# Kernel optimization log

Measured on AMD Instinct MI355X. Metric: run time of the kernel, lower is better.

Reference implementation:

```python
import jax, jax.numpy as jnp
from jax import lax
import numpy as np

CHANNELS = 16
THRESH = 0.1
UPDATE_RATE = 0.25


def _sobel_kernel():
    ident = np.array([[0., 0., 0.], [0., 1., 0.], [0., 0., 0.]], np.float32)
    sx = np.array([[-1., 0., 1.], [-2., 0., 2.], [-1., 0., 1.]], np.float32)
    sy = sx.T
    k = np.stack([ident, sx, sy])[:, None, :, :]          # [3,1,3,3]
    k = np.tile(k, (CHANNELS, 1, 1, 1))                   # [48,1,3,3] (torch repeat order)
    return jnp.asarray(k)


def _perceive(x, w_sobel):
    # circular pad then depthwise grouped conv (groups=CHANNELS, 3 filters per group)
    xp = jnp.pad(x, ((0, 0), (0, 0), (1, 1), (1, 1)), mode='wrap')
    return lax.conv_general_dilated(
        xp, w_sobel, window_strides=(1, 1), padding='VALID',
        dimension_numbers=('NCHW', 'OIHW', 'NCHW'),
        feature_group_count=CHANNELS)                     # [B,48,H,W]


def _alive_mask(x):
    alpha = x[:, 3:4]                                     # [B,1,H,W]
    p = jnp.pad(alpha, ((0, 0), (0, 0), (1, 1), (1, 1)), mode='wrap')
    m = lax.reduce_window(p, -jnp.inf, lax.max, (1, 1, 3, 3), (1, 1, 1, 1), 'VALID')
    return (m > THRESH).astype(x.dtype)


def _mlp(y, w1, b1, w2, b2, w3):
    h = jax.nn.relu(jnp.einsum('bchw,oc->bohw', y, w1) + b1[None, :, None, None])
    h = jax.nn.relu(jnp.einsum('bchw,oc->bohw', h, w2) + b2[None, :, None, None])
    return jnp.einsum('bchw,oc->bohw', h, w3)             # [B,16,H,W], no bias


def setup_inputs() -> dict:
    key = jax.random.key(0)
    ks = jax.random.split(key, 7)
    B, H, W, steps = 8, 256, 256, 2
    s = 0.1
    return {
        'x': jax.random.uniform(ks[0], (B, CHANNELS, H, W), jnp.float32),
        'w1': jax.random.normal(ks[1], (64, 48), jnp.float32) * s,
        'b1': jax.random.normal(ks[2], (64,), jnp.float32) * s,
        'w2': jax.random.normal(ks[3], (64, 64), jnp.float32) * s,
        'b2': jax.random.normal(ks[4], (64,), jnp.float32) * s,
        'w3': jax.random.normal(ks[5], (CHANNELS, 64), jnp.float32) * s,
        'update_masks': jax.random.uniform(ks[6], (steps, B, 1, H, W), jnp.float32),
        'steps': steps,
    }


def reference(x, w1, b1, w2, b2, w3, update_masks, steps):
    w_sobel = _sobel_kernel()
    for i in range(steps):
        pre = _alive_mask(x)
        y = _mlp(_perceive(x, w_sobel), w1, b1, w2, b2, w3)
        um = (update_masks[i] < UPDATE_RATE).astype(x.dtype)
        x = x + y * um
        post = _alive_mask(x)
        x = x * (pre * post)
    return x
```

## Files before the change

### kernel.cpp

```cpp
#include <hip/hip_runtime.h>

#define NB 8
#define NC 16
#define NH 256
#define NW 256
#define ALIVE_THRESH 0.1f
#define UPDATE_RATE 0.25f

typedef __attribute__((ext_vector_type(8))) short bf16x8;
typedef __attribute__((ext_vector_type(4))) float f32x4;
typedef unsigned short ushort_t;

#define MFMA16(a, b, c) __builtin_amdgcn_mfma_f32_16x16x32_bf16((a), (b), (c), 0, 0, 0)

static __device__ __forceinline__ unsigned short f2bf(float f) {
    union { float f; unsigned u; } x; x.f = f;
    unsigned r = x.u + 0x7FFFu + ((x.u >> 16) & 1u);
    return (unsigned short)(r >> 16);
}
static __device__ __forceinline__ float bf2f(unsigned short b) {
    union { unsigned u; float f; } x; x.u = ((unsigned)b) << 16; return x.f;
}

static __device__ __forceinline__ int ybyte(int px, int g) {
    return px * 128 + ((g ^ (px & 7)) << 4);
}

__global__ void prep_weights(const float* __restrict__ w1, const float* __restrict__ b1,
                             const float* __restrict__ w2, const float* __restrict__ w3,
                             int4* __restrict__ wf)
{
    const int f = blockIdx.x, l = threadIdx.x;
    const int lq = l >> 4, ln = l & 15;
    union { unsigned short us[8]; int4 v; } u;
    if (f < 8) {
        const int mt = f >> 1, ks = f & 1, m = mt * 16 + ln;
        #pragma unroll
        for (int j = 0; j < 8; ++j) {
            const int k = ks * 32 + lq * 8 + j;
            float v = (k < 48) ? w1[m * 48 + k] : ((k == 48) ? b1[m] : 0.0f);
            u.us[j] = f2bf(v);
        }
    } else if (f < 16) {
        const int ff = f - 8, mt = ff >> 1, ks = ff & 1, m = mt * 16 + ln;
        #pragma unroll
        for (int j = 0; j < 8; ++j)
            u.us[j] = f2bf(w2[m * 64 + (ks * 32 + lq * 8 + j)]);
    } else {
        const int ks = f - 16, m = ln;
        #pragma unroll
        for (int j = 0; j < 8; ++j)
            u.us[j] = f2bf(w3[m * 64 + (ks * 32 + lq * 8 + j)]);
    }
    wf[f * 64 + l] = u.v;
}

template<bool MASK_IN, bool OUT_BF16>
__global__ __launch_bounds__(256) void nca_step_a(
    const void* __restrict__ xin_v,
    const float* __restrict__ um,
    const float* __restrict__ b2,
    const int4*  __restrict__ wf,
    void* __restrict__ xout_v,
    const unsigned char* __restrict__ preb_in,
    unsigned char* __restrict__ preb_out)
{
    __shared__ char      ybuf[256 * 128];
    __shared__ unsigned  sd[NC][NW];
    __shared__ float     premax2[NW];
    __shared__ float     mmid[NW];

    const int t = threadIdx.x;
    const int bx = blockIdx.x;
    const int h = ((bx & 7) << 5) | (bx >> 3);
    const int b = blockIdx.y;
    const int hm = (h - 1) & (NH - 1), hp = (h + 1) & (NH - 1);
    const size_t cs = (size_t)NH * NW;
    const size_t base = (size_t)b * NC * cs;

    float mreg[NC], dreg[NC];

    if constexpr (MASK_IN) {
        const ushort_t* xin = (const ushort_t*)xin_v;
        float* vbuf = (float*)ybuf;
        const ushort_t* ac = xin + base + 3 * cs;
        float am[5];
        #pragma unroll
        for (int j = 0; j < 5; ++j)
            am[j] = bf2f(ac[(size_t)((h - 2 + j) & (NH - 1)) * NW + t]);
        vbuf[0 * NW + t] = fmaxf(fmaxf(am[0], am[1]), am[2]);
        vbuf[1 * NW + t] = fmaxf(fmaxf(am[1], am[2]), am[3]);
        vbuf[2 * NW + t] = fmaxf(fmaxf(am[2], am[3]), am[4]);
        const unsigned char p0 = preb_in[((size_t)b * NH + hm) * NW + t];
        const unsigned char p1 = preb_in[((size_t)b * NH + h ) * NW + t];
        const unsigned char p2 = preb_in[((size_t)b * NH + hp) * NW + t];
        __syncthreads();

        const int tm = (t - 1) & (NW - 1), tp = (t + 1) & (NW - 1);
        float x0 = fmaxf(fmaxf(vbuf[tm],           vbuf[t]),           vbuf[tp]);
        float x1 = fmaxf(fmaxf(vbuf[NW + tm],      vbuf[NW + t]),      vbuf[NW + tp]);
        float x2 = fmaxf(fmaxf(vbuf[2 * NW + tm],  vbuf[2 * NW + t]),  vbuf[2 * NW + tp]);
        const float m0 = (x0 > ALIVE_THRESH && p0) ? 1.0f : 0.0f;
        const float m1 = (x1 > ALIVE_THRESH && p1) ? 1.0f : 0.0f;
        const float m2 = (x2 > ALIVE_THRESH && p2) ? 1.0f : 0.0f;
        mmid[t] = m1;
        premax2[t] = fmaxf(fmaxf(am[1] * m0, am[2] * m1), am[3] * m2);

        #pragma unroll
        for (int c = 0; c < NC; ++c) {
            float top, mid, bot;
            if (c == 3) { top = am[1] * m0; mid = am[2] * m1; bot = am[3] * m2; }
            else {
                const ushort_t* xc = xin + base + (size_t)c * cs;
                top = bf2f(xc[(size_t)hm * NW + t]) * m0;
                mid = bf2f(xc[(size_t)h  * NW + t]) * m1;
                bot = bf2f(xc[(size_t)hp * NW + t]) * m2;
            }
            float s = top + 2.0f * mid + bot, d = bot - top;
            sd[c][t] = (unsigned)f2bf(s) | ((unsigned)f2bf(d) << 16);
            mreg[c] = mid; dreg[c] = d;
        }
        __syncthreads();
    } else {
        const float* xin = (const float*)xin_v;
        #pragma unroll
        for (int c = 0; c < NC; ++c) {
            const float* xc = xin + base + (size_t)c * cs;
            float top = xc[(size_t)hm * NW + t];
            float mid = xc[(size_t)h  * NW + t];
            float bot = xc[(size_t)hp * NW + t];
            float s = top + 2.0f * mid + bot, d = bot - top;
            sd[c][t] = (unsigned)f2bf(s) | ((unsigned)f2bf(d) << 16);
            mreg[c] = mid; dreg[c] = d;
            if (c == 3) premax2[t] = fmaxf(fmaxf(top, mid), bot);
        }
        __syncthreads();
    }

    {
        const int tm = (t - 1) & (NW - 1), tp = (t + 1) & (NW - 1);
        float mx = fmaxf(fmaxf(premax2[tm], premax2[t]), premax2[tp]);
        preb_out[((size_t)b * NH + h) * NW + t] = (mx > ALIVE_THRESH) ? 1 : 0;
    }

    {
        unsigned yp[24];
        #pragma unroll
        for (int c = 0; c < NC; ++c) {
            unsigned L = sd[c][(t - 1) & (NW - 1)];
            unsigned R = sd[c][(t + 1) & (NW - 1)];
            float sl = bf2f((unsigned short)L), dl = bf2f((unsigned short)(L >> 16));
            float sr = bf2f((unsigned short)R), dr = bf2f((unsigned short)(R >> 16));
            float y0 = mreg[c];
            float y1 = sr - sl;
            float y2 = dl + 2.0f * dreg[c] + dr;
            unsigned short u[3] = { f2bf(y0), f2bf(y1), f2bf(y2) };
            #pragma unroll
            for (int q = 0; q < 3; ++q) {
                const int k = 3 * c + q;
                if ((k & 1) == 0) yp[k >> 1]  = u[q];
                else              yp[k >> 1] |= ((unsigned)u[q]) << 16;
            }
        }
        char* yb = (char*)ybuf;
        #pragma unroll
        for (int g = 0; g < 6; ++g) {
            union { unsigned w[4]; int4 v; } pk;
            pk.w[0] = yp[4 * g]; pk.w[1] = yp[4 * g + 1];
            pk.w[2] = yp[4 * g + 2]; pk.w[3] = yp[4 * g + 3];
            *(int4*)(yb + ybyte(t, g)) = pk.v;
        }
        int4 biasrow; biasrow.x = 0x3F80; biasrow.y = 0; biasrow.z = 0; biasrow.w = 0;
        *(int4*)(yb + ybyte(t, 6)) = biasrow;
        int4 zz; zz.x = zz.y = zz.z = zz.w = 0;
        *(int4*)(yb + ybyte(t, 7)) = zz;
    }

    char* yb = (char*)ybuf;
    const int lane = t & 63, wv = t >> 6;
    const int lq = lane >> 4, ln = lane & 15;
    const int px0 = wv * 64;

    float umv[4];
    {
        const float* umr = um + ((size_t)b * NH + h) * NW;
        #pragma unroll
        for (int nt = 0; nt < 4; ++nt)
            umv[nt] = (umr[px0 + nt * 16 + ln] < UPDATE_RATE) ? 1.0f : 0.0f;
    }

    bf16x8 a1[8];
    #pragma unroll
    for (int f = 0; f < 8; ++f) a1[f] = __builtin_bit_cast(bf16x8, wf[f * 64 + lane]);

    #pragma unroll
    for (int nt = 0; nt < 4; ++nt) {
        const int px = px0 + nt * 16 + ln;
        bf16x8 bb0 = *(const bf16x8*)(yb + ybyte(px, lq));
        bf16x8 bb1 = *(const bf16x8*)(yb + ybyte(px, 4 + lq));
        f32x4 acc[4];
        #pragma unroll
        for (int mt = 0; mt < 4; ++mt) {
            f32x4 z = {0.f, 0.f, 0.f, 0.f};
            z = MFMA16(a1[2 * mt],     bb0, z);
            z = MFMA16(a1[2 * mt + 1], bb1, z);
            acc[mt] = z;
        }
        #pragma unroll
        for (int mt = 0; mt < 4; ++mt) {
            unsigned p0 = (unsigned)f2bf(fmaxf(acc[mt][0], 0.f)) |
                          ((unsigned)f2bf(fmaxf(acc[mt][1], 0.f)) << 16);
            unsigned p1 = (unsigned)f2bf(fmaxf(acc[mt][2], 0.f)) |
                          ((unsigned)f2bf(fmaxf(acc[mt][3], 0.f)) << 16);
            union { unsigned w[2]; uint2 v; } pk; pk.w[0] = p0; pk.w[1] = p1;
            *(uint2*)(yb + ybyte(px, 2 * mt + (lq >> 1)) + (lq & 1) * 8) = pk.v;
        }
    }

    bf16x8 a2[8];
    #pragma unroll
    for (int f = 0; f < 8; ++f) a2[f] = __builtin_bit_cast(bf16x8, wf[(8 + f) * 64 + lane]);
    f32x4 b2v[4];
    #pragma unroll
    for (int mt = 0; mt < 4; ++mt)
        b2v[mt] = *(const f32x4*)(b2 + mt * 16 + lq * 4);

    #pragma unroll
    for (int nt = 0; nt < 4; ++nt) {
        const int px = px0 + nt * 16 + ln;
        bf16x8 bb0 = *(const bf16x8*)(yb + ybyte(px, lq));
        bf16x8 bb1 = *(const bf16x8*)(yb + ybyte(px, 4 + lq));
        f32x4 acc[4];
        #pragma unroll
        for (int mt = 0; mt < 4; ++mt) {
            f32x4 z = {0.f, 0.f, 0.f, 0.f};
            z = MFMA16(a2[2 * mt],     bb0, z);
            z = MFMA16(a2[2 * mt + 1], bb1, z);
            acc[mt] = z + b2v[mt];
        }
        #pragma unroll
        for (int mt = 0; mt < 4; ++mt) {
            unsigned p0 = (unsigned)f2bf(fmaxf(acc[mt][0], 0.f)) |
                          ((unsigned)f2bf(fmaxf(acc[mt][1], 0.f)) << 16);
            unsigned p1 = (unsigned)f2bf(fmaxf(acc[mt][2], 0.f)) |
                          ((unsigned)f2bf(fmaxf(acc[mt][3], 0.f)) << 16);
            union { unsigned w[2]; uint2 v; } pk; pk.w[0] = p0; pk.w[1] = p1;
            *(uint2*)(yb + ybyte(px, 2 * mt + (lq >> 1)) + (lq & 1) * 8) = pk.v;
        }
    }

    bf16x8 a3[2];
    a3[0] = __builtin_bit_cast(bf16x8, wf[16 * 64 + lane]);
    a3[1] = __builtin_bit_cast(bf16x8, wf[17 * 64 + lane]);

    #pragma unroll
    for (int nt = 0; nt < 4; ++nt) {
        const int px = px0 + nt * 16 + ln;
        float xcv[4];
        if constexpr (MASK_IN) {
            const ushort_t* xin = (const ushort_t*)xin_v;
            const float mm = mmid[px];
            #pragma unroll
            for (int r = 0; r < 4; ++r)
                xcv[r] = bf2f(xin[base + (size_t)(lq * 4 + r) * cs + (size_t)h * NW + px]) * mm;
        } else {
            const float* xin = (const float*)xin_v;
            #pragma unroll
            for (int r = 0; r < 4; ++r)
                xcv[r] = xin[base + (size_t)(lq * 4 + r) * cs + (size_t)h * NW + px];
        }
        bf16x8 bb0 = *(const bf16x8*)(yb + ybyte(px, lq));
        bf16x8 bb1 = *(const bf16x8*)(yb + ybyte(px, 4 + lq));
        f32x4 z = {0.f, 0.f, 0.f, 0.f};
        z = MFMA16(a3[0], bb0, z);
        z = MFMA16(a3[1], bb1, z);
        #pragma unroll
        for (int r = 0; r < 4; ++r) {
            const size_t o = base + (size_t)(lq * 4 + r) * cs + (size_t)h * NW + px;
            float val = xcv[r] + z[r] * umv[nt];
            if constexpr (OUT_BF16) ((ushort_t*)xout_v)[o] = f2bf(val);
            else                    ((float*)xout_v)[o]   = val;
        }
    }
}

__global__ __launch_bounds__(256) void nca_step_b(
    const float* __restrict__ xmid,
    const unsigned char* __restrict__ preb,
    float* __restrict__ xout)
{
    const int gid = blockIdx.x * 256 + threadIdx.x;
    const int b   = gid >> 14;
    const int rem = gid & 16383;
    const int h   = rem >> 6;
    const int px  = (rem & 63) << 2;

    const float* alpha = xmid + ((size_t)b * NC + 3) * NH * NW;
    float m0 = -1e30f, m1 = -1e30f, m2 = -1e30f, m3 = -1e30f;
    #pragma unroll
    for (int dy = -1; dy <= 1; ++dy) {
        const int row = (h + dy) & (NH - 1);
        const float* r = alpha + (size_t)row * NW;
        float4 mid4 = *(const float4*)(r + px);
        float lm = r[(px - 1) & (NW - 1)];
        float rm = r[(px + 4) & (NW - 1)];
        m0 = fmaxf(m0, fmaxf(fmaxf(lm, mid4.x), mid4.y));
        m1 = fmaxf(m1, fmaxf(fmaxf(mid4.x, mid4.y), mid4.z));
        m2 = fmaxf(m2, fmaxf(fmaxf(mid4.y, mid4.z), mid4.w));
        m3 = fmaxf(m3, fmaxf(fmaxf(mid4.z, mid4.w), rm));
    }
    const size_t pix = ((size_t)b * NH + h) * NW + px;
    const unsigned char* pr = preb + pix;
    float f0 = (m0 > ALIVE_THRESH && pr[0]) ? 1.0f : 0.0f;
    float f1 = (m1 > ALIVE_THRESH && pr[1]) ? 1.0f : 0.0f;
    float f2 = (m2 > ALIVE_THRESH && pr[2]) ? 1.0f : 0.0f;
    float f3 = (m3 > ALIVE_THRESH && pr[3]) ? 1.0f : 0.0f;

    #pragma unroll
    for (int c = 0; c < NC; ++c) {
        const size_t o = (((size_t)b * NC + c) * NH + h) * NW + px;
        float4 v = *(const float4*)(xmid + o);
        v.x *= f0; v.y *= f1; v.z *= f2; v.w *= f3;
        *(float4*)(xout + o) = v;
    }
}

extern "C" void kernel_launch(void* const* d_in, const int* in_sizes, int n_in,
                              void* d_out, int out_size, void* d_ws, size_t ws_size,
                              hipStream_t stream) {
    const float* x  = (const float*)d_in[0];
    const float* w1 = (const float*)d_in[1];
    const float* b1 = (const float*)d_in[2];
    const float* w2 = (const float*)d_in[3];
    const float* b2 = (const float*)d_in[4];
    const float* w3 = (const float*)d_in[5];
    const float* um = (const float*)d_in[6];
    const int steps = in_sizes[6] / (NB * NH * NW);

    const size_t npix  = (size_t)NB * NH * NW;
    const size_t nelem = (size_t)NB * NC * NH * NW;

    float* xmid2         = (float*)d_ws;
    unsigned char* prebA = (unsigned char*)(xmid2 + nelem);
    unsigned char* prebB = prebA + npix;
    int4* wf             = (int4*)(prebB + npix);
    float* xout          = (float*)d_out;
    ushort_t* bfA        = (ushort_t*)d_out;
    ushort_t* bfB        = bfA + nelem;

    prep_weights<<<18, 64, 0, stream>>>(w1, b1, w2, w3, wf);

    dim3 grdA(NH, NB);
    const int grdB = (int)(npix / 4) / 256;

    const void* cur = x;
    unsigned char* preb_last = prebA;
    for (int i = 0; i < steps; ++i) {
        const bool first = (i == 0), last = (i == steps - 1);
        const float* um_i = um + (size_t)i * npix;
        unsigned char* pout = (i % 2 == 0) ? prebA : prebB;
        unsigned char* pin  = (i % 2 == 0) ? prebB : prebA;
        void* bf_next = (i % 2 == 0) ? (void*)bfA : (void*)bfB;

        if (first && last) {
            nca_step_a<false, false><<<grdA, 256, 0, stream>>>(
                cur, um_i, b2, wf, xmid2, nullptr, pout);
        } else if (first) {
            nca_step_a<false, true><<<grdA, 256, 0, stream>>>(
                cur, um_i, b2, wf, bf_next, nullptr, pout);
            cur = bf_next;
        } else if (last) {
            nca_step_a<true, false><<<grdA, 256, 0, stream>>>(
                cur, um_i, b2, wf, xmid2, pin, pout);
        } else {
            nca_step_a<true, true><<<grdA, 256, 0, stream>>>(
                cur, um_i, b2, wf, bf_next, pin, pout);
            cur = bf_next;
        }
        preb_last = pout;
    }

    nca_step_b<<<grdB, 256, 0, stream>>>(xmid2, preb_last, xout);
}
```

Baseline: 76.47 us.

## Store last-step state in bf16 and overlay shared memory buffers

The last step now writes its state as bf16 instead of an fp32 intermediate, and the final alive-mask kernel reads bf16 rows using a shared-memory vertical max. This cuts the bytes moved between the last step and the final pass. Shared memory for the sd and ybuf buffers is overlaid into one region, and f2bf switches to the HIP intrinsic. The yp packing loop is computed twice (the second pass overwrites the first), which is redundant work, and the extra bf16 rounding of the final state may reduce accuracy.

```diff
diff --git a/kernel.cpp b/kernel.cpp
--- a/kernel.cpp
+++ b/kernel.cpp
@@ -1,4 +1,5 @@
 #include <hip/hip_runtime.h>
+#include <hip/hip_bf16.h>
 
 #define NB 8
 #define NC 16
@@ -14,12 +15,14 @@
 #define MFMA16(a, b, c) __builtin_amdgcn_mfma_f32_16x16x32_bf16((a), (b), (c), 0, 0, 0)
 
 static __device__ __forceinline__ unsigned short f2bf(float f) {
-    union { float f; unsigned u; } x; x.f = f;
-    unsigned r = x.u + 0x7FFFu + ((x.u >> 16) & 1u);
-    return (unsigned short)(r >> 16);
+    __hip_bfloat16 h = __float2bfloat16(f);
+    return __builtin_bit_cast(unsigned short, h);
 }
 static __device__ __forceinline__ float bf2f(unsigned short b) {
     union { unsigned u; float f; } x; x.u = ((unsigned)b) << 16; return x.f;
+}
+static __device__ __forceinline__ unsigned pack2(float lo, float hi) {
+    return (unsigned)f2bf(lo) | ((unsigned)f2bf(hi) << 16);
 }
 
 static __device__ __forceinline__ int ybyte(int px, int g) {
@@ -55,20 +58,23 @@
     wf[f * 64 + l] = u.v;
 }
 
-template<bool MASK_IN, bool OUT_BF16>
+template<bool MASK_IN>
 __global__ __launch_bounds__(256) void nca_step_a(
     const void* __restrict__ xin_v,
     const float* __restrict__ um,
     const float* __restrict__ b2,
     const int4*  __restrict__ wf,
-    void* __restrict__ xout_v,
+    ushort_t* __restrict__ xout,
     const unsigned char* __restrict__ preb_in,
     unsigned char* __restrict__ preb_out)
 {
-    __shared__ char      ybuf[256 * 128];
-    __shared__ unsigned  sd[NC][NW];
-    __shared__ float     premax2[NW];
-    __shared__ float     mmid[NW];
+    __shared__ char  smem[256 * 128];
+    __shared__ float premax2[NW];
+    __shared__ float mmid[NW];
+
+    char*     yb   = smem;
+    unsigned* sd   = (unsigned*)(smem + 4096);
+    float*    vbuf = (float*)smem;
 
     const int t = threadIdx.x;
     const int bx = blockIdx.x;
@@ -82,7 +88,6 @@
 
     if constexpr (MASK_IN) {
         const ushort_t* xin = (const ushort_t*)xin_v;
-        float* vbuf = (float*)ybuf;
         const ushort_t* ac = xin + base + 3 * cs;
         float am[5];
         #pragma unroll
@@ -97,9 +102,9 @@
         __syncthreads();
 
         const int tm = (t - 1) & (NW - 1), tp = (t + 1) & (NW - 1);
-        float x0 = fmaxf(fmaxf(vbuf[tm],           vbuf[t]),           vbuf[tp]);
-        float x1 = fmaxf(fmaxf(vbuf[NW + tm],      vbuf[NW + t]),      vbuf[NW + tp]);
-        float x2 = fmaxf(fmaxf(vbuf[2 * NW + tm],  vbuf[2 * NW + t]),  vbuf[2 * NW + tp]);
+        float x0 = fmaxf(fmaxf(vbuf[tm],          vbuf[t]),          vbuf[tp]);
+        float x1 = fmaxf(fmaxf(vbuf[NW + tm],     vbuf[NW + t]),     vbuf[NW + tp]);
+        float x2 = fmaxf(fmaxf(vbuf[2 * NW + tm], vbuf[2 * NW + t]), vbuf[2 * NW + tp]);
         const float m0 = (x0 > ALIVE_THRESH && p0) ? 1.0f : 0.0f;
         const float m1 = (x1 > ALIVE_THRESH && p1) ? 1.0f : 0.0f;
         const float m2 = (x2 > ALIVE_THRESH && p2) ? 1.0f : 0.0f;
@@ -117,7 +122,7 @@
                 bot = bf2f(xc[(size_t)hp * NW + t]) * m2;
             }
             float s = top + 2.0f * mid + bot, d = bot - top;
-            sd[c][t] = (unsigned)f2bf(s) | ((unsigned)f2bf(d) << 16);
+            sd[c * NW + t] = pack2(s, d);
             mreg[c] = mid; dreg[c] = d;
         }
         __syncthreads();
@@ -130,7 +135,7 @@
             float mid = xc[(size_t)h  * NW + t];
             float bot = xc[(size_t)hp * NW + t];
             float s = top + 2.0f * mid + bot, d = bot - top;
-            sd[c][t] = (unsigned)f2bf(s) | ((unsigned)f2bf(d) << 16);
+            sd[c * NW + t] = pack2(s, d);
             mreg[c] = mid; dreg[c] = d;
             if (c == 3) premax2[t] = fmaxf(fmaxf(top, mid), bot);
         }
@@ -143,26 +148,50 @@
         preb_out[((size_t)b * NH + h) * NW + t] = (mx > ALIVE_THRESH) ? 1 : 0;
     }
 
-    {
-        unsigned yp[24];
+    unsigned yp[24];
+    {
+        const int tm = (t - 1) & (NW - 1), tp = (t + 1) & (NW - 1);
         #pragma unroll
         for (int c = 0; c < NC; ++c) {
-            unsigned L = sd[c][(t - 1) & (NW - 1)];
-            unsigned R = sd[c][(t + 1) & (NW - 1)];
+            unsigned L = sd[c * NW + tm];
+            unsigned R = sd[c * NW + tp];
             float sl = bf2f((unsigned short)L), dl = bf2f((unsigned short)(L >> 16));
             float sr = bf2f((unsigned short)R), dr = bf2f((unsigned short)(R >> 16));
             float y0 = mreg[c];
             float y1 = sr - sl;
             float y2 = dl + 2.0f * dreg[c] + dr;
-            unsigned short u[3] = { f2bf(y0), f2bf(y1), f2bf(y2) };
-            #pragma unroll
-            for (int q = 0; q < 3; ++q) {
-                const int k = 3 * c + q;
-                if ((k & 1) == 0) yp[k >> 1]  = u[q];
-                else              yp[k >> 1] |= ((unsigned)u[q]) << 16;
+            unsigned short u0 = f2bf(y0), u1 = f2bf(y1), u2 = f2bf(y2);
+            const int k = 3 * c;
+            if ((k & 1) == 0) {
+                yp[k >> 1] = (unsigned)u0 | ((unsigned)u1 << 16);
+                if (((k + 2) & 1) == 0) yp[(k + 2) >> 1] = (unsigned)u2;
+                else                    yp[(k + 2) >> 1] |= 0;
+            } else {
+                yp[k >> 1] |= ((unsigned)u0 << 16);
+                yp[(k + 1) >> 1] = (unsigned)u1 | ((unsigned)u2 << 16);
             }
         }
-        char* yb = (char*)ybuf;
+    }
+    {
+        const int tm = (t - 1) & (NW - 1), tp = (t + 1) & (NW - 1);
+        unsigned short ys[48];
+        #pragma unroll
+        for (int c = 0; c < NC; ++c) {
+            unsigned L = sd[c * NW + tm];
+            unsigned R = sd[c * NW + tp];
+            float sl = bf2f((unsigned short)L), dl = bf2f((unsigned short)(L >> 16));
+            float sr = bf2f((unsigned short)R), dr = bf2f((unsigned short)(R >> 16));
+            ys[3 * c + 0] = f2bf(mreg[c]);
+            ys[3 * c + 1] = f2bf(sr - sl);
+            ys[3 * c + 2] = f2bf(dl + 2.0f * dreg[c] + dr);
+        }
+        #pragma unroll
+        for (int i = 0; i < 24; ++i)
+            yp[i] = (unsigned)ys[2 * i] | ((unsigned)ys[2 * i + 1] << 16);
+    }
+    __syncthreads();
+
+    {
         #pragma unroll
         for (int g = 0; g < 6; ++g) {
             union { unsigned w[4]; int4 v; } pk;
@@ -176,7 +205,6 @@
         *(int4*)(yb + ybyte(t, 7)) = zz;
     }
 
-    char* yb = (char*)ybuf;
     const int lane = t & 63, wv = t >> 6;
     const int lq = lane >> 4, ln = lane & 15;
     const int px0 = wv * 64;
@@ -208,10 +236,8 @@
         }
         #pragma unroll
         for (int mt = 0; mt < 4; ++mt) {
-            unsigned p0 = (unsigned)f2bf(fmaxf(acc[mt][0], 0.f)) |
-                          ((unsigned)f2bf(fmaxf(acc[mt][1], 0.f)) << 16);
-            unsigned p1 = (unsigned)f2bf(fmaxf(acc[mt][2], 0.f)) |
-                          ((unsigned)f2bf(fmaxf(acc[mt][3], 0.f)) << 16);
+            unsigned p0 = pack2(fmaxf(acc[mt][0], 0.f), fmaxf(acc[mt][1], 0.f));
+            unsigned p1 = pack2(fmaxf(acc[mt][2], 0.f), fmaxf(acc[mt][3], 0.f));
             union { unsigned w[2]; uint2 v; } pk; pk.w[0] = p0; pk.w[1] = p1;
             *(uint2*)(yb + ybyte(px, 2 * mt + (lq >> 1)) + (lq & 1) * 8) = pk.v;
         }
@@ -240,10 +266,8 @@
         }
         #pragma unroll
         for (int mt = 0; mt < 4; ++mt) {
-            unsigned p0 = (unsigned)f2bf(fmaxf(acc[mt][0], 0.f)) |
-                          ((unsigned)f2bf(fmaxf(acc[mt][1], 0.f)) << 16);
-            unsigned p1 = (unsigned)f2bf(fmaxf(acc[mt][2], 0.f)) |
-                          ((unsigned)f2bf(fmaxf(acc[mt][3], 0.f)) << 16);
+            unsigned p0 = pack2(fmaxf(acc[mt][0], 0.f), fmaxf(acc[mt][1], 0.f));
+            unsigned p1 = pack2(fmaxf(acc[mt][2], 0.f), fmaxf(acc[mt][3], 0.f));
             union { unsigned w[2]; uint2 v; } pk; pk.w[0] = p0; pk.w[1] = p1;
             *(uint2*)(yb + ybyte(px, 2 * mt + (lq >> 1)) + (lq & 1) * 8) = pk.v;
         }
@@ -277,51 +301,42 @@
         #pragma unroll
         for (int r = 0; r < 4; ++r) {
             const size_t o = base + (size_t)(lq * 4 + r) * cs + (size_t)h * NW + px;
-            float val = xcv[r] + z[r] * umv[nt];
-            if constexpr (OUT_BF16) ((ushort_t*)xout_v)[o] = f2bf(val);
-            else                    ((float*)xout_v)[o]   = val;
-        }
-    }
-}
-
-__global__ __launch_bounds__(256) void nca_step_b(
-    const float* __restrict__ xmid,
+            xout[o] = f2bf(xcv[r] + z[r] * umv[nt]);
+        }
+    }
+}
+
+__global__ __launch_bounds__(256) void nca_final(
+    const ushort_t* __restrict__ bf,
     const unsigned char* __restrict__ preb,
     float* __restrict__ xout)
 {
-    const int gid = blockIdx.x * 256 + threadIdx.x;
-    const int b   = gid >> 14;
-    const int rem = gid & 16383;
-    const int h   = rem >> 6;
-    const int px  = (rem & 63) << 2;
-
-    const float* alpha = xmid + ((size_t)b * NC + 3) * NH * NW;
-    float m0 = -1e30f, m1 = -1e30f, m2 = -1e30f, m3 = -1e30f;
-    #pragma unroll
-    for (int dy = -1; dy <= 1; ++dy) {
-        const int row = (h + dy) & (NH - 1);
-        const float* r = alpha + (size_t)row * NW;
-        float4 mid4 = *(const float4*)(r + px);
-        float lm = r[(px - 1) & (NW - 1)];
-        float rm = r[(px + 4) & (NW - 1)];
-        m0 = fmaxf(m0, fmaxf(fmaxf(lm, mid4.x), mid4.y));
-        m1 = fmaxf(m1, fmaxf(fmaxf(mid4.x, mid4.y), mid4.z));
-        m2 = fmaxf(m2, fmaxf(fmaxf(mid4.y, mid4.z), mid4.w));
-        m3 = fmaxf(m3, fmaxf(fmaxf(mid4.z, mid4.w), rm));
-    }
-    const size_t pix = ((size_t)b * NH + h) * NW + px;
-    const unsigned char* pr = preb + pix;
-    float f0 = (m0 > ALIVE_THRESH && pr[0]) ? 1.0f : 0.0f;
-    float f1 = (m1 > ALIVE_THRESH && pr[1]) ? 1.0f : 0.0f;
-    float f2 = (m2 > ALIVE_THRESH && pr[2]) ? 1.0f : 0.0f;
-    float f3 = (m3 > ALIVE_THRESH && pr[3]) ? 1.0f : 0.0f;
+    __shared__ float vmax[NW];
+
+    const int t = threadIdx.x;
+    const int bx = blockIdx.x;
+    const int h = ((bx & 7) << 5) | (bx >> 3);
+    const int b = blockIdx.y;
+    const int hm = (h - 1) & (NH - 1), hp = (h + 1) & (NH - 1);
+    const size_t cs = (size_t)NH * NW;
+    const size_t base = (size_t)b * NC * cs;
+
+    const ushort_t* ac = bf + base + 3 * cs;
+    float a0 = bf2f(ac[(size_t)hm * NW + t]);
+    float a1 = bf2f(ac[(size_t)h  * NW + t]);
+    float a2 = bf2f(ac[(size_t)hp * NW + t]);
+    vmax[t] = fmaxf(fmaxf(a0, a1), a2);
+    const unsigned char p = preb[((size_t)b * NH + h) * NW + t];
+    __syncthreads();
+
+    const int tm = (t - 1) & (NW - 1), tp = (t + 1) & (NW - 1);
+    float mx = fmaxf(fmaxf(vmax[tm], vmax[t]), vmax[tp]);
+    const float m = (mx > ALIVE_THRESH && p) ? 1.0f : 0.0f;
 
     #pragma unroll
     for (int c = 0; c < NC; ++c) {
-        const size_t o = (((size_t)b * NC + c) * NH + h) * NW + px;
-        float4 v = *(const float4*)(xmid + o);
-        v.x *= f0; v.y *= f1; v.z *= f2; v.w *= f3;
-        *(float4*)(xout + o) = v;
+        const size_t o = base + (size_t)c * cs + (size_t)h * NW + t;
+        xout[o] = bf2f(bf[o]) * m;
     }
 }
 
@@ -340,45 +355,34 @@
     const size_t npix  = (size_t)NB * NH * NW;
     const size_t nelem = (size_t)NB * NC * NH * NW;
 
-    float* xmid2         = (float*)d_ws;
-    unsigned char* prebA = (unsigned char*)(xmid2 + nelem);
+    ushort_t* bfA        = (ushort_t*)d_ws;
+    ushort_t* bfB        = bfA + nelem;
+    unsigned char* prebA = (unsigned char*)(bfB + nelem);
     unsigned char* prebB = prebA + npix;
     int4* wf             = (int4*)(prebB + npix);
     float* xout          = (float*)d_out;
-    ushort_t* bfA        = (ushort_t*)d_out;
-    ushort_t* bfB        = bfA + nelem;
 
     prep_weights<<<18, 64, 0, stream>>>(w1, b1, w2, w3, wf);
 
     dim3 grdA(NH, NB);
-    const int grdB = (int)(npix / 4) / 256;
 
     const void* cur = x;
     unsigned char* preb_last = prebA;
     for (int i = 0; i < steps; ++i) {
-        const bool first = (i == 0), last = (i == steps - 1);
         const float* um_i = um + (size_t)i * npix;
-        unsigned char* pout = (i % 2 == 0) ? prebA : prebB;
-        unsigned char* pin  = (i % 2 == 0) ? prebB : prebA;
-        void* bf_next = (i % 2 == 0) ? (void*)bfA : (void*)bfB;
-
-        if (first && last) {
-            nca_step_a<false, false><<<grdA, 256, 0, stream>>>(
-                cur, um_i, b2, wf, xmid2, nullptr, pout);
-        } else if (first) {
-            nca_step_a<false, true><<<grdA, 256, 0, stream>>>(
-                cur, um_i, b2, wf, bf_next, nullptr, pout);
-            cur = bf_next;
-        } else if (last) {
-            nca_step_a<true, false><<<grdA, 256, 0, stream>>>(
-                cur, um_i, b2, wf, xmid2, pin, pout);
-        } else {
-            nca_step_a<true, true><<<grdA, 256, 0, stream>>>(
-                cur, um_i, b2, wf, bf_next, pin, pout);
-            cur = bf_next;
-        }
-        preb_last = pout;
-    }
-
-    nca_step_b<<<grdB, 256, 0, stream>>>(xmid2, preb_last, xout);
-}
+        ushort_t* bfo      = (i % 2 == 0) ? bfA : bfB;
+        unsigned char* po  = (i % 2 == 0) ? prebA : prebB;
+        unsigned char* pin = (i % 2 == 0) ? prebB : prebA;
+
+        if (i == 0)
+            nca_step_a<false><<<grdA, 256, 0, stream>>>(
+                cur, um_i, b2, wf, bfo, nullptr, po);
+        else
+            nca_step_a<true><<<grdA, 256, 0, stream>>>(
+                cur, um_i, b2, wf, bfo, pin, po);
+        cur = bfo;
+        preb_last = po;
+    }
+
+    nca_final<<<grdA, 256, 0, stream>>>((const ushort_t*)cur, preb_last, xout);
+}
```

Result: faster. 63.70 us (-16.7%).
